# Performance work log

Measured on AMD Instinct MI355X. Metric: run time of the kernel, lower is better.

The kernel has to match this reference:

```python
import jax, jax.numpy as jnp
import numpy as np

D_MODEL = 1024
NHEAD = 16
HEAD_DIM = D_MODEL // NHEAD
ROPE_BASE = 10000.0


def _rope_freq(T, head_dim):
    half = head_dim // 2
    pos = jnp.arange(T, dtype=jnp.float32)
    idx = jnp.arange(half, dtype=jnp.float32)
    freq_div = ROPE_BASE ** (2.0 * idx / head_dim)
    return pos[:, None] / freq_div[None, :]  # [T, half]


def _rope_rotate(x, cos, sin):
    # x: [B, H, T, d]; cos/sin: [T, d//2]
    half = x.shape[-1] // 2
    xl, xr = x[..., :half], x[..., half:]
    c = cos[None, None]
    s = sin[None, None]
    return jnp.concatenate([xl * c - xr * s, xl * s + xr * c], axis=-1)


def setup_inputs() -> dict:
    key = jax.random.key(0)
    ks = jax.random.split(key, 12)
    B, T = 2, 2048
    sd = 1.0 / np.sqrt(D_MODEL)
    inp = {
        "query": jax.random.normal(ks[0], (B, T, D_MODEL), jnp.float32),
        "key": jax.random.normal(ks[1], (B, T, D_MODEL), jnp.float32),
        "value": jax.random.normal(ks[2], (B, T, D_MODEL), jnp.float32),
        "frac": jax.random.uniform(ks[3], (B, T), jnp.float32),
        # Linear weights stored [in, out] (torch W.T)
        "Wq": jax.random.normal(ks[4], (D_MODEL, D_MODEL), jnp.float32) * sd,
        "Wk": jax.random.normal(ks[5], (D_MODEL, D_MODEL), jnp.float32) * sd,
        "Wv": jax.random.normal(ks[6], (D_MODEL, D_MODEL), jnp.float32) * sd,
        "Wo": jax.random.normal(ks[7], (D_MODEL, D_MODEL), jnp.float32) * sd,
        "bq": jnp.zeros((D_MODEL,), jnp.float32),
        "bk": jnp.zeros((D_MODEL,), jnp.float32),
        "bv": jnp.zeros((D_MODEL,), jnp.float32),
        "bo": jnp.zeros((D_MODEL,), jnp.float32),
        "alpha_pos": jax.random.normal(ks[8], (NHEAD,), jnp.float32) * 0.1,
        "alpha_neg": jax.random.normal(ks[9], (NHEAD,), jnp.float32) * 0.1,
    }
    return inp


def reference(query, key, value, frac, Wq, Wk, Wv, Wo, bq, bk, bv, bo, alpha_pos, alpha_neg):
    B, T, dm = query.shape
    H, hd = NHEAD, HEAD_DIM
    scale = hd ** -0.5

    def split_heads(x):  # [B,T,dm] -> [B,H,T,hd]
        return x.reshape(B, T, H, hd).transpose(0, 2, 1, 3)

    Q = split_heads(query @ Wq + bq)
    K = split_heads(key @ Wk + bk)
    V = split_heads(value @ Wv + bv)

    freq = _rope_freq(T, hd)
    cos, sin = jnp.cos(freq), jnp.sin(freq)
    Q = _rope_rotate(Q, cos, sin)
    K = _rope_rotate(K, cos, sin)

    scores = jnp.einsum("bhqd,bhkd->bhqk", Q, K) * scale  # [B,H,T,T]

    # data-dependent stoichiometric bias
    D = frac[:, None, :] - frac[:, :, None]  # [B,T,T], D[b,i,j] = frac_j - frac_i
    D_pos = jax.nn.relu(D)
    D_neg = -jax.nn.relu(-D)
    bias = (alpha_pos[None, :, None, None] * D_pos[:, None] +
            alpha_neg[None, :, None, None] * D_neg[:, None])  # [B,H,T,T]
    scores = scores + bias

    probs = jax.nn.softmax(scores, axis=-1)
    out = jnp.einsum("bhqk,bhkd->bhqd", probs, V)  # [B,H,T,hd]
    out = out.transpose(0, 2, 1, 3).reshape(B, T, dm)
    return out @ Wo + bo
```

## Files before the change

### kernel.cpp

```cpp
#include <hip/hip_runtime.h>


typedef unsigned short u16;
typedef __bf16 bf8v __attribute__((ext_vector_type(8)));
typedef __bf16 bf4v __attribute__((ext_vector_type(4)));
typedef float f32x4 __attribute__((ext_vector_type(4)));

#define D_MODEL 1024
#define T_SEQ   2048
#define NHEAD   16
#define HDIM    64
#define BATCH   2
#define M_TOT   (BATCH * T_SEQ)
#define LOG2E   1.4426950408889634f

__device__ __forceinline__ void gl2lds16(const u16* g, u16* l) {
  __builtin_amdgcn_global_load_lds(
      (__attribute__((address_space(1))) void*)g,
      (__attribute__((address_space(3))) void*)l, 16, 0, 0);
}

__global__ __launch_bounds__(256) void k_prep(
    const float* __restrict__ q, const float* __restrict__ k,
    const float* __restrict__ v, const float* __restrict__ Wq,
    const float* __restrict__ Wk, const float* __restrict__ Wv,
    const float* __restrict__ Wo, u16* __restrict__ Xb, u16* __restrict__ WtB,
    float* __restrict__ ct, float* __restrict__ st) {
  __shared__ float tile[64 * 65];
  int bx = blockIdx.x, tid = threadIdx.x;
  if (bx < 6144) {
    int z = bx >> 11, xb = bx & 2047;
    const float* src = (z == 0) ? q : (z == 1) ? k : v;
    u16* dst = Xb + (size_t)z * (M_TOT * D_MODEL);
    int idx = (xb * 256 + tid) * 8;
    float4 a = *(const float4*)(src + idx);
    float4 b = *(const float4*)(src + idx + 4);
    bf8v o;
    o[0] = (__bf16)a.x; o[1] = (__bf16)a.y; o[2] = (__bf16)a.z; o[3] = (__bf16)a.w;
    o[4] = (__bf16)b.x; o[5] = (__bf16)b.y; o[6] = (__bf16)b.z; o[7] = (__bf16)b.w;
    *(bf8v*)(dst + idx) = o;
  } else if (bx < 7168) {
    int idx2 = bx - 6144;
    int z = idx2 >> 8, rem = idx2 & 255;
    int k0 = (rem >> 4) * 64, n0 = (rem & 15) * 64;
    const float* W = (z == 0) ? Wq : (z == 1) ? Wk : (z == 2) ? Wv : Wo;
    u16* Wt = WtB + (size_t)z * (D_MODEL * D_MODEL);
#pragma unroll
    for (int i = 0; i < 16; i++) {
      int idx = tid + i * 256;
      int r = idx >> 6, c = idx & 63;
      tile[c * 65 + r] = W[(size_t)(k0 + r) * D_MODEL + n0 + c];
    }
    __syncthreads();
#pragma unroll
    for (int i = 0; i < 16; i++) {
      int idx = tid + i * 256;
      int r = idx >> 6, c = idx & 63;
      ((__bf16*)Wt)[(size_t)(n0 + r) * D_MODEL + k0 + c] = (__bf16)tile[r * 65 + c];
    }
  } else {
    int idx = (bx - 7168) * 256 + tid;
    int t = idx >> 5, d = idx & 31;
    float ang = (float)t * powf(10000.0f, -(float)d * (1.0f / 32.0f));
    ct[idx] = cosf(ang);
    st[idx] = sinf(ang);
  }
}

__device__ __forceinline__ void gemm_core_128(const u16* __restrict__ A,
                                              const u16* __restrict__ Bt,
                                              u16* sA, u16* sB,
                                              f32x4 (&acc)[4][4],
                                              int m0, int n0) {
  const int K = D_MODEL;
  int tid = threadIdx.x;
  int lane = tid & 63, wave = tid >> 6;
  int l15 = lane & 15, quad = lane >> 4;
  int wm = (wave >> 1) * 64, wn = (wave & 1) * 64;
  int r0 = tid >> 2, pcol0 = (tid & 3) * 8;
  int r1 = 64 + r0;
  const u16* A0 = A + (size_t)(m0 + r0) * K + pcol0;
  const u16* A1 = A + (size_t)(m0 + r1) * K + pcol0;
  const u16* B0 = Bt + (size_t)(n0 + r0) * K + pcol0;
  const u16* B1 = Bt + (size_t)(n0 + r1) * K + pcol0;
  u16* dA0 = sA + wave * 512;
  u16* dA1 = sA + 2048 + wave * 512;
  u16* dB0 = sB + wave * 512;
  u16* dB1 = sB + 2048 + wave * 512;
  for (int k0 = 0; k0 < K; k0 += 64) {
    __syncthreads();
    gl2lds16(A0 + k0, dA0);
    gl2lds16(A1 + k0, dA1);
    gl2lds16(A0 + k0 + 32, dA0 + 4096);
    gl2lds16(A1 + k0 + 32, dA1 + 4096);
    gl2lds16(B0 + k0, dB0);
    gl2lds16(B0 + k0 + 32, dB0 + 4096);
    gl2lds16(B1 + k0, dB1);
    gl2lds16(B1 + k0 + 32, dB1 + 4096);
    __syncthreads();
#pragma unroll
    for (int kh = 0; kh < 2; kh++) {
      bf8v af[4], bf[4];
#pragma unroll
      for (int i = 0; i < 4; i++)
        af[i] = *(const bf8v*)(sA + kh * 4096 + (wm + i * 16 + l15) * 32 + quad * 8);
#pragma unroll
      for (int i = 0; i < 4; i++)
        bf[i] = *(const bf8v*)(sB + kh * 4096 + (wn + i * 16 + l15) * 32 + quad * 8);
#pragma unroll
      for (int mi = 0; mi < 4; mi++)
#pragma unroll
        for (int ni = 0; ni < 4; ni++)
          acc[mi][ni] = __builtin_amdgcn_mfma_f32_16x16x32_bf16(
              af[mi], bf[ni], acc[mi][ni], 0, 0, 0);
    }
  }
}

__global__ __launch_bounds__(256) void k_gemm_qkv(
    const u16* __restrict__ Xb, const u16* __restrict__ WtB,
    const float* __restrict__ bq, const float* __restrict__ bk,
    const float* __restrict__ bv, const float* __restrict__ ctab,
    const float* __restrict__ stab, u16* __restrict__ OutB,
    u16* __restrict__ Vb) {
  __shared__ __align__(16) u16 sA[128 * 64];
  __shared__ __align__(16) u16 sB[128 * 64];
  int z = blockIdx.z;
  const u16* A = Xb + (size_t)z * (M_TOT * D_MODEL);
  const u16* Bt = WtB + (size_t)z * (D_MODEL * D_MODEL);
  const float* bias = (z == 0) ? bq : (z == 1) ? bk : bv;
  u16* Out = OutB + (size_t)z * (M_TOT * D_MODEL);
  int m0 = blockIdx.y * 128, n0 = blockIdx.x * 128;
  f32x4 acc[4][4] = {};
  gemm_core_128(A, Bt, sA, sB, acc, m0, n0);

  int tid = threadIdx.x, lane = tid & 63, wave = tid >> 6;
  int l15 = lane & 15, quad = lane >> 4;
  int wm = (wave >> 1) * 64, wn = (wave & 1) * 64;
  float bvv[4];
#pragma unroll
  for (int ni = 0; ni < 4; ni++) bvv[ni] = bias[n0 + wn + ni * 16 + l15];

  if (z < 2) {
    float qs = (z == 0) ? 0.125f * LOG2E : 1.0f;
#pragma unroll
    for (int mi = 0; mi < 4; mi++) {
#pragma unroll
      for (int r = 0; r < 4; r++) {
        int m = m0 + wm + mi * 16 + quad * 4 + r;
        size_t ro = (size_t)m * D_MODEL + n0 + wn;
        int tl = m & (T_SEQ - 1);
#pragma unroll
        for (int ni = 0; ni < 2; ni++) {
          int d = ni * 16 + l15;
          float c = ctab[tl * 32 + d], s = stab[tl * 32 + d];
          float xl = acc[mi][ni][r] + bvv[ni];
          float xr = acc[mi][ni + 2][r] + bvv[ni + 2];
          ((__bf16*)Out)[ro + d] = (__bf16)((xl * c - xr * s) * qs);
          ((__bf16*)Out)[ro + d + 32] = (__bf16)((xl * s + xr * c) * qs);
        }
      }
    }
  } else {
    int hh = (n0 + wn) >> 6;
    int mbase = m0 + wm;
    int bb = mbase >> 11;
    int tbase = mbase & (T_SEQ - 1);
    u16* Vw = Vb + (size_t)(bb * NHEAD + hh) * HDIM * T_SEQ;
#pragma unroll
    for (int mi = 0; mi < 4; mi++)
#pragma unroll
      for (int r = 0; r < 4; r++) {
        int t = tbase + mi * 16 + quad * 4 + r;
#pragma unroll
        for (int ni = 0; ni < 4; ni++) {
          int d = ni * 16 + l15;
          ((__bf16*)Vw)[(size_t)d * T_SEQ + t] = (__bf16)(acc[mi][ni][r] + bvv[ni]);
        }
      }
  }
}

__global__ __launch_bounds__(256) void k_gemm_out(
    const u16* __restrict__ ctx, const u16* __restrict__ Wot,
    const float* __restrict__ bo, float* __restrict__ Cout) {
  __shared__ __align__(16) u16 sA[64 * 64];
  __shared__ __align__(16) u16 sB[64 * 64];
  const int K = D_MODEL;
  int m0 = blockIdx.y * 64, n0 = blockIdx.x * 64;
  int tid = threadIdx.x, lane = tid & 63, wave = tid >> 6;
  int l15 = lane & 15, quad = lane >> 4;
  int wm = (wave >> 1) * 32, wn = (wave & 1) * 32;
  int r0 = tid >> 2, pcol0 = (tid & 3) * 8;
  const u16* A0 = ctx + (size_t)(m0 + r0) * K + pcol0;
  const u16* B0 = Wot + (size_t)(n0 + r0) * K + pcol0;
  u16* dA = sA + wave * 512;
  u16* dB = sB + wave * 512;
  f32x4 acc[2][2] = {};
  for (int k0 = 0; k0 < K; k0 += 64) {
    __syncthreads();
    gl2lds16(A0 + k0, dA);
    gl2lds16(A0 + k0 + 32, dA + 2048);
    gl2lds16(B0 + k0, dB);
    gl2lds16(B0 + k0 + 32, dB + 2048);
    __syncthreads();
#pragma unroll
    for (int kh = 0; kh < 2; kh++) {
      bf8v af[2], bf[2];
#pragma unroll
      for (int i = 0; i < 2; i++)
        af[i] = *(const bf8v*)(sA + kh * 2048 + (wm + i * 16 + l15) * 32 + quad * 8);
#pragma unroll
      for (int i = 0; i < 2; i++)
        bf[i] = *(const bf8v*)(sB + kh * 2048 + (wn + i * 16 + l15) * 32 + quad * 8);
#pragma unroll
      for (int mi = 0; mi < 2; mi++)
#pragma unroll
        for (int ni = 0; ni < 2; ni++)
          acc[mi][ni] = __builtin_amdgcn_mfma_f32_16x16x32_bf16(
              af[mi], bf[ni], acc[mi][ni], 0, 0, 0);
    }
  }
  float bvv[2];
#pragma unroll
  for (int ni = 0; ni < 2; ni++) bvv[ni] = bo[n0 + wn + ni * 16 + l15];
#pragma unroll
  for (int mi = 0; mi < 2; mi++)
#pragma unroll
    for (int r = 0; r < 4; r++) {
      size_t ro = (size_t)(m0 + wm + mi * 16 + quad * 4 + r) * D_MODEL + n0 + wn;
#pragma unroll
      for (int ni = 0; ni < 2; ni++)
        Cout[ro + ni * 16 + l15] = acc[mi][ni][r] + bvv[ni];
    }
}

__global__ __launch_bounds__(512, 4) void k_attn(
    const u16* __restrict__ Qr, const u16* __restrict__ Kr,
    const u16* __restrict__ Vb, const float* __restrict__ frac,
    const float* __restrict__ alpha_pos, const float* __restrict__ alpha_neg,
    u16* __restrict__ ctx) {
  __shared__ __align__(16) u16 smem[26624];
  int bh = blockIdx.y, b = bh >> 4, h = bh & 15;
  int q0 = blockIdx.x * 128;
  int tid = threadIdx.x, wave = tid >> 6, lane = tid & 63;
  int l15 = lane & 15, quad = lane >> 4;
  int qw = wave & 3;
  int kh = wave >> 2;

  const u16* Kh = Kr + (size_t)b * T_SEQ * D_MODEL + h * HDIM;
  const u16* Vh = Vb + (size_t)bh * HDIM * T_SEQ;
  const float* fb = frac + b * T_SEQ;

  bf8v qf[2][2];
  float fq[2];
#pragma unroll
  for (int g = 0; g < 2; g++) {
    int qrow = q0 + qw * 32 + g * 16 + l15;
    const u16* qbase =
        Qr + (size_t)(b * T_SEQ + qrow) * D_MODEL + h * HDIM + quad * 8;
    qf[g][0] = *(const bf8v*)qbase;
    qf[g][1] = *(const bf8v*)(qbase + 32);
    fq[g] = fb[qrow];
  }
  float ap = alpha_pos[h] * LOG2E, an = alpha_neg[h] * LOG2E;
  float c1 = 0.5f * (ap + an), c2 = 0.5f * (ap - an);
  bf8v onesv;
#pragma unroll
  for (int j = 0; j < 8; j++) onesv[j] = (__bf16)1.0f;
  f32x4 o[2][4] = {};
  f32x4 o_l[2] = {};
  u16* kT0 = smem;
  u16* vT0 = smem + 8192;
  u16* pw = smem + 16384 + wave * 1280;

  int x0 = (quad ^ (l15 & 7)) * 8;
  int kidx[2], vidx[4];
#pragma unroll
  for (int nt = 0; nt < 2; nt++)
    kidx[nt] = (((kh * 2 + nt) * 16 + l15) << 6) + x0;
#pragma unroll
  for (int dt = 0; dt < 4; dt++)
    vidx[dt] = (((dt * 16 + l15) << 6) + x0) ^ (kh * 32);
  int pidx = l15 * 40 + quad * 8;

  int kr0 = tid >> 3, gc0 = (tid & 7) ^ (kr0 & 7);
  const u16* kg0 = Kh + (size_t)kr0 * D_MODEL + gc0 * 8;
  const u16* vg0 = Vh + (size_t)kr0 * T_SEQ + gc0 * 8;
  int woff = wave * 512;

  auto stage = [&](int buf, int kbase) {
    gl2lds16(kg0 + (size_t)kbase * D_MODEL, kT0 + buf * 4096 + woff);
    gl2lds16(vg0 + kbase, vT0 + buf * 4096 + woff);
  };

  stage(0, 0);
  __syncthreads();

  for (int kt = 0; kt < T_SEQ / 64; kt++) {
    int kbase = kt * 64;
    int buf = kt & 1;
    if (kt + 1 < T_SEQ / 64) stage(buf ^ 1, kbase + 64);
    const u16* kb = kT0 + buf * 4096;
    const u16* vb = vT0 + buf * 4096;

    bf8v kf0[2], kf1[2];
#pragma unroll
    for (int nt = 0; nt < 2; nt++) {
      kf0[nt] = *(const bf8v*)(kb + kidx[nt]);
      kf1[nt] = *(const bf8v*)(kb + (kidx[nt] ^ 32));
    }
    bf8v vf[4];
#pragma unroll
    for (int dt = 0; dt < 4; dt++) vf[dt] = *(const bf8v*)(vb + vidx[dt]);
    f32x4 fk4[2];
#pragma unroll
    for (int nt = 0; nt < 2; nt++)
      fk4[nt] = *(const f32x4*)(fb + kbase + kh * 32 + nt * 16 + quad * 4);

#pragma unroll
    for (int g = 0; g < 2; g++) {
      float fqg = fq[g];
      u16* pwg = pw + g * 640;
#pragma unroll
      for (int nt = 0; nt < 2; nt++) {
        f32x4 s = {};
        s = __builtin_amdgcn_mfma_f32_16x16x32_bf16(kf0[nt], qf[g][0], s, 0, 0, 0);
        s = __builtin_amdgcn_mfma_f32_16x16x32_bf16(kf1[nt], qf[g][1], s, 0, 0, 0);
        bf4v pk;
#pragma unroll
        for (int r = 0; r < 4; r++) {
          float dd = fk4[nt][r] - fqg;
          pk[r] = (__bf16)__builtin_amdgcn_exp2f(
              fmaf(c2, __builtin_fabsf(dd), fmaf(c1, dd, s[r])));
        }
        *(bf4v*)(pwg + l15 * 40 + nt * 16 + quad * 4) = pk;
      }
      asm volatile("s_waitcnt lgkmcnt(0)" ::: "memory");
      bf8v pf = *(const bf8v*)(pwg + pidx);
      o_l[g] = __builtin_amdgcn_mfma_f32_16x16x32_bf16(pf, onesv, o_l[g], 0, 0, 0);
#pragma unroll
      for (int dt = 0; dt < 4; dt++)
        o[g][dt] = __builtin_amdgcn_mfma_f32_16x16x32_bf16(pf, vf[dt],
                                                           o[g][dt], 0, 0, 0);
    }
    __syncthreads();
  }

  float* Of = (float*)smem;
  float* Lf = (float*)(smem + 26368);
  if (kh == 1) {
#pragma unroll
    for (int g = 0; g < 2; g++)
#pragma unroll
      for (int r = 0; r < 4; r++) {
        int ql = qw * 32 + g * 16 + quad * 4 + r;
#pragma unroll
        for (int dt = 0; dt < 4; dt++)
          Of[ql * 66 + dt * 16 + l15] = o[g][dt][r];
        if (l15 == 0) Lf[ql] = o_l[g][r];
      }
  }
  __syncthreads();
  if (kh == 0) {
#pragma unroll
    for (int g = 0; g < 2; g++)
#pragma unroll
      for (int r = 0; r < 4; r++) {
        int ql = qw * 32 + g * 16 + quad * 4 + r;
        float linv = 1.0f / (o_l[g][r] + Lf[ql]);
        __bf16* orow =
            (__bf16*)(ctx + (size_t)(b * T_SEQ + q0 + ql) * D_MODEL + h * HDIM);
#pragma unroll
        for (int dt = 0; dt < 4; dt++)
          orow[dt * 16 + l15] =
              (__bf16)((o[g][dt][r] + Of[ql * 66 + dt * 16 + l15]) * linv);
      }
  }
}

extern "C" void kernel_launch(void* const* d_in, const int* in_sizes, int n_in,
                              void* d_out, int out_size, void* d_ws,
                              size_t ws_size, hipStream_t stream) {
  const float* q = (const float*)d_in[0];
  const float* k = (const float*)d_in[1];
  const float* v = (const float*)d_in[2];
  const float* frac = (const float*)d_in[3];
  const float* Wq = (const float*)d_in[4];
  const float* Wk = (const float*)d_in[5];
  const float* Wv = (const float*)d_in[6];
  const float* Wo = (const float*)d_in[7];
  const float* bq = (const float*)d_in[8];
  const float* bk = (const float*)d_in[9];
  const float* bv = (const float*)d_in[10];
  const float* bo = (const float*)d_in[11];
  const float* alpha_pos = (const float*)d_in[12];
  const float* alpha_neg = (const float*)d_in[13];

  char* ws = (char*)d_ws;
  u16* Xb = (u16*)(ws + 0);
  u16* Wt = (u16*)(ws + 25165824);
  u16* Qr = (u16*)(ws + 33554432);
  u16* Kr = (u16*)(ws + 41943040);
  u16* Vtmp = (u16*)(ws + 50331648);
  u16* Vb = (u16*)(ws + 58720256);
  float* ctab = (float*)(ws + 67108864);
  float* stab = (float*)(ws + 67371008);
  u16* ctx = Vtmp;
  u16* QKVout = Qr;

  k_prep<<<dim3(7424), 256, 0, stream>>>(q, k, v, Wq, Wk, Wv, Wo, Xb, Wt, ctab,
                                         stab);
  k_gemm_qkv<<<dim3(8, 32, 3), 256, 0, stream>>>(Xb, Wt, bq, bk, bv, ctab, stab,
                                                 QKVout, Vb);
  k_attn<<<dim3(16, 32), 512, 0, stream>>>(Qr, Kr, Vb, frac, alpha_pos,
                                           alpha_neg, ctx);
  k_gemm_out<<<dim3(16, 64), 256, 0, stream>>>(ctx, Wt + 3 * 1048576, bo,
                                               (float*)d_out);
}
```

Before: 240.0 us.

## Triple-buffer K/V tiles in attention with one barrier, XCD-aware block remap

Replaces the double-buffered K/V staging with a three-buffer ring that prefetches two tiles ahead. It syncs with vmcnt waits plus a single barrier per iteration instead of a trailing __syncthreads. It also caches the per-batch frac vector in LDS, raises wave priority around the MFMA sections, and remaps block indices so all blocks of one head land on the same XCD for L2 reuse. This trades more LDS per block, which may reduce occupancy, for better latency hiding and less global traffic.

```diff
diff --git a/kernel.cpp b/kernel.cpp
--- a/kernel.cpp
+++ b/kernel.cpp
@@ -240,9 +240,12 @@
     const u16* __restrict__ Vb, const float* __restrict__ frac,
     const float* __restrict__ alpha_pos, const float* __restrict__ alpha_neg,
     u16* __restrict__ ctx) {
-  __shared__ __align__(16) u16 smem[26624];
-  int bh = blockIdx.y, b = bh >> 4, h = bh & 15;
-  int q0 = blockIdx.x * 128;
+  __shared__ __align__(16) u16 smem[38912];
+  int lin = blockIdx.x + (blockIdx.y << 4);
+  int xcd = lin & 7, slot = lin >> 3;
+  int bh = (xcd << 2) | (slot >> 4);
+  int q0 = (slot & 15) << 7;
+  int b = bh >> 4, h = bh & 15;
   int tid = threadIdx.x, wave = tid >> 6, lane = tid & 63;
   int l15 = lane & 15, quad = lane >> 4;
   int qw = wave & 3;
@@ -251,6 +254,11 @@
   const u16* Kh = Kr + (size_t)b * T_SEQ * D_MODEL + h * HDIM;
   const u16* Vh = Vb + (size_t)bh * HDIM * T_SEQ;
   const float* fb = frac + b * T_SEQ;
+
+  u16* kT0 = smem;
+  u16* vT0 = smem + 12288;
+  u16* pw = smem + 24576 + wave * 1280;
+  float* fl = (float*)(smem + 34816);
 
   bf8v qf[2][2];
   float fq[2];
@@ -263,6 +271,11 @@
     qf[g][1] = *(const bf8v*)(qbase + 32);
     fq[g] = fb[qrow];
   }
+  {
+    f32x4 fv = *(const f32x4*)(fb + (tid << 2));
+    *(f32x4*)(fl + (tid << 2)) = fv;
+  }
+
   float ap = alpha_pos[h] * LOG2E, an = alpha_neg[h] * LOG2E;
   float c1 = 0.5f * (ap + an), c2 = 0.5f * (ap - an);
   bf8v onesv;
@@ -270,9 +283,6 @@
   for (int j = 0; j < 8; j++) onesv[j] = (__bf16)1.0f;
   f32x4 o[2][4] = {};
   f32x4 o_l[2] = {};
-  u16* kT0 = smem;
-  u16* vT0 = smem + 8192;
-  u16* pw = smem + 16384 + wave * 1280;
 
   int x0 = (quad ^ (l15 & 7)) * 8;
   int kidx[2], vidx[4];
@@ -289,20 +299,28 @@
   const u16* vg0 = Vh + (size_t)kr0 * T_SEQ + gc0 * 8;
   int woff = wave * 512;
 
-  auto stage = [&](int buf, int kbase) {
-    gl2lds16(kg0 + (size_t)kbase * D_MODEL, kT0 + buf * 4096 + woff);
-    gl2lds16(vg0 + kbase, vT0 + buf * 4096 + woff);
+  auto stage = [&](int bufoff, int kbase) {
+    gl2lds16(kg0 + (size_t)kbase * D_MODEL, kT0 + bufoff + woff);
+    gl2lds16(vg0 + kbase, vT0 + bufoff + woff);
   };
 
   stage(0, 0);
-  __syncthreads();
-
+  stage(4096, 64);
+  asm volatile("s_waitcnt lgkmcnt(0)" ::: "memory");
+
+  int oc = 0, o1 = 4096, o2 = 8192;
   for (int kt = 0; kt < T_SEQ / 64; kt++) {
     int kbase = kt * 64;
-    int buf = kt & 1;
-    if (kt + 1 < T_SEQ / 64) stage(buf ^ 1, kbase + 64);
-    const u16* kb = kT0 + buf * 4096;
-    const u16* vb = vT0 + buf * 4096;
+    if (kt == T_SEQ / 64 - 1)
+      asm volatile("s_waitcnt vmcnt(0)" ::: "memory");
+    else
+      asm volatile("s_waitcnt vmcnt(2)" ::: "memory");
+    __builtin_amdgcn_s_barrier();
+    asm volatile("" ::: "memory");
+    __builtin_amdgcn_sched_barrier(0);
+    if (kt + 2 < T_SEQ / 64) stage(o2, kbase + 128);
+    const u16* kb = kT0 + oc;
+    const u16* vb = vT0 + oc;
 
     bf8v kf0[2], kf1[2];
 #pragma unroll
@@ -316,7 +334,7 @@
     f32x4 fk4[2];
 #pragma unroll
     for (int nt = 0; nt < 2; nt++)
-      fk4[nt] = *(const f32x4*)(fb + kbase + kh * 32 + nt * 16 + quad * 4);
+      fk4[nt] = *(const f32x4*)(fl + kbase + kh * 32 + nt * 16 + quad * 4);
 
 #pragma unroll
     for (int g = 0; g < 2; g++) {
@@ -325,8 +343,10 @@
 #pragma unroll
       for (int nt = 0; nt < 2; nt++) {
         f32x4 s = {};
+        __builtin_amdgcn_s_setprio(1);
         s = __builtin_amdgcn_mfma_f32_16x16x32_bf16(kf0[nt], qf[g][0], s, 0, 0, 0);
         s = __builtin_amdgcn_mfma_f32_16x16x32_bf16(kf1[nt], qf[g][1], s, 0, 0, 0);
+        __builtin_amdgcn_s_setprio(0);
         bf4v pk;
 #pragma unroll
         for (int r = 0; r < 4; r++) {
@@ -338,17 +358,20 @@
       }
       asm volatile("s_waitcnt lgkmcnt(0)" ::: "memory");
       bf8v pf = *(const bf8v*)(pwg + pidx);
+      __builtin_amdgcn_s_setprio(1);
       o_l[g] = __builtin_amdgcn_mfma_f32_16x16x32_bf16(pf, onesv, o_l[g], 0, 0, 0);
 #pragma unroll
       for (int dt = 0; dt < 4; dt++)
         o[g][dt] = __builtin_amdgcn_mfma_f32_16x16x32_bf16(pf, vf[dt],
                                                            o[g][dt], 0, 0, 0);
-    }
-    __syncthreads();
-  }
+      __builtin_amdgcn_s_setprio(0);
+    }
+    int tmp = oc; oc = o1; o1 = o2; o2 = tmp;
+  }
+  __syncthreads();
 
   float* Of = (float*)smem;
-  float* Lf = (float*)(smem + 26368);
+  float* Lf = (float*)(smem + 16896);
   if (kh == 1) {
 #pragma unroll
     for (int g = 0; g < 2; g++)
```

New measurement: 238.0 us. No clear change (-0.8%).
